# Kernel tuning notes

Hardware: AMD Instinct MI355X
Metric: run time of the kernel (lower is better)

The kernel has to match this reference:

```python
import jax, jax.numpy as jnp
import numpy as np

B, T, M, E, H = 8, 1024, 8192, 1024, 128
DECAY = 0.01
LQ_ADD = 1e-4
POS_TABLE_SIZE = 32


def setup_inputs() -> dict:
    key = jax.random.key(0)
    ks = jax.random.split(key, 9)
    return {
        "block_pos_list": jax.random.randint(ks[0], (B,), 0, 10),
        "inp": jax.random.normal(ks[1], (B, T, E), jnp.float32),
        "memory": jax.random.normal(ks[2], (B, M, E), jnp.float32),
        "memory_block_dist": jax.random.randint(ks[3], (B, M), 0, 1000).astype(jnp.int32),
        "memory_rank": jax.random.normal(ks[4], (B, M), jnp.float32),
        "pos_table": jax.random.normal(ks[5], (POS_TABLE_SIZE, E), jnp.float32) * 0.02,
        "Wk": jax.random.normal(ks[6], (H, E), jnp.float32) / np.float32(np.sqrt(E)),
        "Wq": jax.random.normal(ks[7], (H, E), jnp.float32) / np.float32(np.sqrt(E)),
        "Wv": jax.random.normal(ks[8], (H, E), jnp.float32) / np.float32(np.sqrt(E)),
    }


def reference(block_pos_list, inp, memory, memory_block_dist, memory_rank, pos_table, Wk, Wq, Wv):
    # --- reset slots where block_pos == 0 (start of a new work) ---
    reset = (block_pos_list == 0)                               # [B]
    memory = jnp.where(reset[:, None, None], 0.0, memory)       # [B, M, E]
    dist = jnp.where(reset[:, None], 0, memory_block_dist) + 1  # [B, M]

    # --- log2-bucketed positional embedding added to memory ---
    m_pos_ix = jnp.floor(jnp.log2(dist.astype(jnp.float32))).astype(jnp.int32)
    m_with_emb = memory + pos_table[m_pos_ix]                   # [B, M, E]
    mk = jnp.concatenate([m_with_emb, inp], axis=1)             # [B, M+T, E]

    # --- projections (torch Linear: x @ W.T) ---
    k = jnp.einsum('bse,he->bsh', mk, Wk)                       # [B, M+T, H]
    q = jnp.einsum('bte,he->bth', inp, Wq)                      # [B, T, H]
    v = jnp.einsum('bse,he->bsh', mk, Wv)                       # [B, M+T, H]

    # --- square + max-normalize attention (not softmax) ---
    mbs = M + T
    wei = jnp.einsum('bth,bsh->bts', q, k) * np.float32(mbs ** -0.5)  # [B, T, M+T]
    wei = wei * wei
    wei = wei / jnp.max(wei, axis=2, keepdims=True)

    # --- per-slot rank update ---
    mean_wei = jnp.mean(jnp.sum(wei, axis=1), axis=1)           # [B]
    new_rank = memory_rank + jnp.sum(wei[:, :, :M], axis=1) / mean_wei[:, None] - 1.0 - DECAY

    # --- sort memory slots by rank (descending), evict bottom block ---
    order = jnp.argsort(-new_rank, axis=1)                      # [B, M]
    mem_s = jnp.take_along_axis(memory, order[:, :, None], axis=1)
    dist_s = jnp.take_along_axis(dist, order, axis=1)
    rank_s = jnp.take_along_axis(new_rank, order, axis=1)
    r = min(T, M)
    new_memory = jax.lax.stop_gradient(mem_s.at[:, -r:].set(inp[:, -r:]))
    new_dist = dist_s.at[:, -r:].set(0)
    new_rank_out = jax.lax.stop_gradient(rank_s.at[:, -r:].set(1.0))

    qt_loss = jnp.sum(jnp.log(wei + LQ_ADD))
    out = jnp.einsum('bts,bsh->bth', wei, v)                    # [B, T, H]
    return out, qt_loss, new_memory, new_dist, new_rank_out
```

## Files before the change

kernel.cpp:

```cpp
#include <hip/hip_runtime.h>
#include <hip/hip_bf16.h>
#include <stdint.h>

#define BB 8
#define TT 1024
#define MM 8192
#define EE 1024
#define HH 128
#define SS (MM + TT)
#define RKEEP (MM - 1024)
#define NSPLIT 8
#define SCHUNK (SS / NSPLIT)
#define NT (SCHUNK / 64)
#define BK 32
#define NKVBLK (SS / 64)

typedef __attribute__((ext_vector_type(8))) short bf16x8;
typedef __attribute__((ext_vector_type(4))) short s16x4;
typedef __attribute__((ext_vector_type(4))) float f32x4;

#define SBAR()   __builtin_amdgcn_s_barrier()
#define SCB()    __builtin_amdgcn_sched_barrier(0)

static __device__ __forceinline__ unsigned f2ord(float f) {
    unsigned u = __float_as_uint(f);
    return u ^ ((u & 0x80000000u) ? 0xFFFFFFFFu : 0x80000000u);
}
static __device__ __forceinline__ float ord2f(unsigned o) {
    unsigned u = (o & 0x80000000u) ? (o ^ 0x80000000u) : ~o;
    return __uint_as_float(u);
}
static __device__ __forceinline__ unsigned short f2bf(float x) {
    unsigned u = __float_as_uint(x);
    unsigned r = u + 0x7FFFu + ((u >> 16) & 1u);
    return (unsigned short)(r >> 16);
}

static __device__ __forceinline__ void gload_lds16(const short* g, short* l) {
    __builtin_amdgcn_global_load_lds(
        (const __attribute__((address_space(1))) void*)g,
        (__attribute__((address_space(3))) void*)l, 16, 0, 0);
}

__device__ const float SCALEF = (float)(1.0 / 96.0);

__global__ __launch_bounds__(256) void k_init(
    const float* __restrict__ Wk, const float* __restrict__ Wq, const float* __restrict__ Wv,
    short* __restrict__ wk, short* __restrict__ wq, short* __restrict__ wv,
    float* __restrict__ outZ, float* __restrict__ rmax)
{
    const int blk = blockIdx.x, tid = threadIdx.x;
    if (blk < 384) {
        int idx = blk * 256 + tid;
        int m = idx >> 15;
        int o4 = (idx & 32767) * 4;
        const float* W = m == 0 ? Wk : (m == 1 ? Wq : Wv);
        short* D = m == 0 ? wk : (m == 1 ? wq : wv);
        f32x4 v = *(const f32x4*)&W[o4];
        s16x4 h;
#pragma unroll
        for (int j = 0; j < 4; ++j) h[j] = (short)f2bf(v[j]);
        *(s16x4*)&D[o4] = h;
    } else {
        const int z = (blk - 384) * 256 + tid;
        const f32x4 zero = (f32x4){0.f, 0.f, 0.f, 0.f};
        for (int i = z; i < (BB * TT * HH) / 4; i += 128 * 256)
            ((f32x4*)outZ)[i] = zero;
        if (z == 0) outZ[BB * TT * HH] = 0.f;
        if (z < (BB * TT) / 4) ((f32x4*)rmax)[z] = zero;
    }
}

__global__ __launch_bounds__(256, 4) void k_proj(
    const float* __restrict__ memory, const int* __restrict__ mbd,
    const int* __restrict__ bpl, const float* __restrict__ pos_table,
    const float* __restrict__ inp,
    const short* __restrict__ wk, const short* __restrict__ wv,
    const short* __restrict__ wq,
    short* __restrict__ kb, short* __restrict__ vT, short* __restrict__ qb)
{
    __shared__ __align__(16) short smA[64 * 64];
    __shared__ __align__(16) short smB[2][2][128 * 32];

    const int tid = threadIdx.x;
    const int b   = blockIdx.y;
    const int lane = tid & 63, wid = tid >> 6;
    const int wc = wid;
    const int fr = lane & 15, fq = lane >> 4;
    const int arow = tid >> 2;
    const int aq   = tid & 3;
    const int wh   = (tid >> 2);
    const int wk8  = (tid & 3) * 8;
    const int wdst = wid * 512;

    if (blockIdx.x < NKVBLK) {
        const int s0 = blockIdx.x * 64;
        const bool reset = (bpl[b] == 0);
        int pix;
        const float* abase;
        {
            int s = s0 + arow;
            if (s < MM) {
                int d = reset ? 1 : (mbd[b * MM + s] + 1);
                pix = 31 - __clz(d);
                abase = reset ? nullptr : &memory[((size_t)b * MM + s) * EE];
            } else {
                pix = -1;
                abase = &inp[((size_t)b * TT + (s - MM)) * EE];
            }
        }

        f32x4 accK[4][2], accV[4][2];
#pragma unroll
        for (int m = 0; m < 4; ++m)
#pragma unroll
            for (int n = 0; n < 2; ++n) {
                accK[m][n] = (f32x4){0.f, 0.f, 0.f, 0.f};
                accV[m][n] = (f32x4){0.f, 0.f, 0.f, 0.f};
            }

        auto STAGEW = [&](int e0, int buf) {
#pragma unroll
            for (int p = 0; p < 2; ++p) {
                int h = p * 64 + wh;
                int ec = wk8 ^ ((h & 3) << 3);
                size_t g = (size_t)h * EE + e0 + ec;
                gload_lds16(&wk[g], &smB[buf][0][p * 2048 + wdst]);
                gload_lds16(&wv[g], &smB[buf][1][p * 2048 + wdst]);
            }
        };
        auto LOADP = [&](int p, f32x4 xa[4]) {
            int e0 = p * 64 + aq * 16;
#pragma unroll
            for (int j = 0; j < 4; ++j) {
                f32x4 v = (f32x4){0.f, 0.f, 0.f, 0.f};
                if (abase) v = *(const f32x4*)&abase[e0 + j * 4];
                if (pix >= 0) {
                    f32x4 pt = *(const f32x4*)&pos_table[(size_t)pix * EE + e0 + j * 4];
                    v[0] += pt[0]; v[1] += pt[1]; v[2] += pt[2]; v[3] += pt[3];
                }
                xa[j] = v;
            }
        };
        auto STOREP = [&](const f32x4 xa[4]) {
#pragma unroll
            for (int j = 0; j < 2; ++j) {
                bf16x8 h;
#pragma unroll
                for (int c = 0; c < 4; ++c) {
                    h[c]     = (short)f2bf(xa[2 * j][c]);
                    h[4 + c] = (short)f2bf(xa[2 * j + 1][c]);
                }
                int g = (aq * 2 + j) ^ (arow & 7);
                *(bf16x8*)&smA[arow * 64 + g * 8] = h;
            }
        };

        f32x4 xa[4];
        LOADP(0, xa);
        STOREP(xa);
        STAGEW(0, 0);
        __syncthreads();
        LOADP(1, xa);

        for (int step = 0; step < 32; ++step) {
            const int wbuf = step & 1;
            const int sseg = step & 1;
            if (step < 31) STAGEW((step + 1) * BK, wbuf ^ 1);

            bf16x8 ah[4];
#pragma unroll
            for (int m = 0; m < 4; ++m) {
                int r = m * 16 + fr;
                int g = (sseg * 4 + fq) ^ (r & 7);
                ah[m] = *(const bf16x8*)&smA[r * 64 + g * 8];
            }
#pragma unroll
            for (int n = 0; n < 2; ++n) {
                int c = wc * 32 + n * 16 + fr;
                int off = c * 32 + ((fq * 8) ^ ((c & 3) << 3));
                bf16x8 kh = *(const bf16x8*)&smB[wbuf][0][off];
                bf16x8 vh = *(const bf16x8*)&smB[wbuf][1][off];
#pragma unroll
                for (int m = 0; m < 4; ++m) {
                    accK[m][n] = __builtin_amdgcn_mfma_f32_16x16x32_bf16(ah[m], kh, accK[m][n], 0, 0, 0);
                    accV[m][n] = __builtin_amdgcn_mfma_f32_16x16x32_bf16(ah[m], vh, accV[m][n], 0, 0, 0);
                }
            }
            __syncthreads();
            if (sseg == 1 && step < 31) {
                STOREP(xa);
                __syncthreads();
                if (step < 29) LOADP((step >> 1) + 2, xa);
            }
        }

#pragma unroll
        for (int m = 0; m < 4; ++m) {
            int row = s0 + m * 16 + fq * 4;
#pragma unroll
            for (int n = 0; n < 2; ++n) {
                int col = wc * 32 + n * 16 + fr;
#pragma unroll
                for (int i = 0; i < 4; ++i)
                    kb[((size_t)b * SS + row + i) * HH + col] = (short)f2bf(accK[m][n][i]);
            }
        }
        float* tpT = (float*)smB;
#pragma unroll
        for (int hp = 0; hp < 4; ++hp) {
            __syncthreads();
            if (wc == hp) {
#pragma unroll
                for (int m = 0; m < 4; ++m)
#pragma unroll
                    for (int n = 0; n < 2; ++n) {
                        int cl = n * 16 + fr;
                        int row = m * 16 + fq * 4;
                        *(f32x4*)&tpT[cl * 68 + row] = accV[m][n];
                    }
            }
            __syncthreads();
            for (int idx = tid; idx < 32 * 16; idx += 256) {
                int hcl = idx >> 4, s4 = (idx & 15) << 2;
                f32x4 v = *(const f32x4*)&tpT[hcl * 68 + s4];
                s16x4 hi;
#pragma unroll
                for (int j = 0; j < 4; ++j) hi[j] = (short)f2bf(v[j]);
                size_t o = ((size_t)b * HH + hp * 32 + hcl) * SS + s0 + s4;
                *(s16x4*)&vT[o] = hi;
            }
        }
    } else {
        const int t0 = (blockIdx.x - NKVBLK) * 64;
        const float* abase = &inp[((size_t)b * TT + t0 + arow) * EE];

        f32x4 acc[4][2];
#pragma unroll
        for (int m = 0; m < 4; ++m)
#pragma unroll
            for (int n = 0; n < 2; ++n) acc[m][n] = (f32x4){0.f, 0.f, 0.f, 0.f};

        auto STAGEWQ = [&](int e0, int buf) {
#pragma unroll
            for (int p = 0; p < 2; ++p) {
                int h = p * 64 + wh;
                int ec = wk8 ^ ((h & 3) << 3);
                size_t g = (size_t)h * EE + e0 + ec;
                gload_lds16(&wq[g], &smB[buf][0][p * 2048 + wdst]);
            }
        };
        auto LOADPQ = [&](int p, f32x4 xa[4]) {
            int e0 = p * 64 + aq * 16;
#pragma unroll
            for (int j = 0; j < 4; ++j) xa[j] = *(const f32x4*)&abase[e0 + j * 4];
        };
        auto STOREPQ = [&](const f32x4 xa[4]) {
#pragma unroll
            for (int j = 0; j < 2; ++j) {
                bf16x8 h;
#pragma unroll
                for (int c = 0; c < 4; ++c) {
                    h[c]     = (short)f2bf(xa[2 * j][c]);
                    h[4 + c] = (short)f2bf(xa[2 * j + 1][c]);
                }
                int g = (aq * 2 + j) ^ (arow & 7);
                *(bf16x8*)&smA[arow * 64 + g * 8] = h;
            }
        };

        f32x4 xa[4];
        LOADPQ(0, xa);
        STOREPQ(xa);
        STAGEWQ(0, 0);
        __syncthreads();
        LOADPQ(1, xa);

        for (int step = 0; step < 32; ++step) {
            const int wbuf = step & 1;
            const int sseg = step & 1;
            if (step < 31) STAGEWQ((step + 1) * BK, wbuf ^ 1);

            bf16x8 ah[4];
#pragma unroll
            for (int m = 0; m < 4; ++m) {
                int r = m * 16 + fr;
                int g = (sseg * 4 + fq) ^ (r & 7);
                ah[m] = *(const bf16x8*)&smA[r * 64 + g * 8];
            }
#pragma unroll
            for (int n = 0; n < 2; ++n) {
                int c = wc * 32 + n * 16 + fr;
                int off = c * 32 + ((fq * 8) ^ ((c & 3) << 3));
                bf16x8 bh = *(const bf16x8*)&smB[wbuf][0][off];
#pragma unroll
                for (int m = 0; m < 4; ++m)
                    acc[m][n] = __builtin_amdgcn_mfma_f32_16x16x32_bf16(ah[m], bh, acc[m][n], 0, 0, 0);
            }
            __syncthreads();
            if (sseg == 1 && step < 31) {
                STOREPQ(xa);
                __syncthreads();
                if (step < 29) LOADPQ((step >> 1) + 2, xa);
            }
        }
#pragma unroll
        for (int m = 0; m < 4; ++m) {
            int row = t0 + m * 16 + fq * 4;
#pragma unroll
            for (int n = 0; n < 2; ++n) {
                int col = wc * 32 + n * 16 + fr;
#pragma unroll
                for (int i = 0; i < 4; ++i)
                    qb[((size_t)b * TT + row + i) * HH + col] = (short)f2bf(acc[m][n][i]);
            }
        }
    }
}

__device__ __forceinline__ void stage_k64_async(const short* __restrict__ src,
                                                size_t rowBase, int tid, short* sh)
{
#pragma unroll
    for (int c2 = 0; c2 < 4; ++c2) {
        int srow = c2 * 16 + (tid >> 4);
        int scol = ((tid & 15) * 8) ^ ((srow & 7) << 3);
        size_t g = (rowBase + srow) * HH + scol;
        gload_lds16(&src[g], &sh[c2 * 2048 + (tid >> 6) * 512]);
    }
}

__device__ __forceinline__ void stage_v64_async(const short* __restrict__ vT,
                                                int b, int st, int tid, short* vs)
{
#pragma unroll
    for (int c2 = 0; c2 < 4; ++c2) {
        int h = c2 * 32 + (tid >> 3);
        int sc = ((tid & 7) * 8) ^ ((h & 7) << 3);
        size_t g = ((size_t)b * HH + h) * SS + st + sc;
        gload_lds16(&vT[g], &vs[c2 * 2048 + (tid >> 6) * 512]);
    }
}

__device__ __forceinline__ void load_qfrags(const short* __restrict__ qb,
                                            size_t rowIx, int fq, bf16x8 qh[4])
{
    size_t base = rowIx * HH + fq * 8;
#pragma unroll
    for (int k = 0; k < 4; ++k)
        qh[k] = *(const bf16x8*)&qb[base + k * 32];
}

__device__ __forceinline__ void qk_mfma4(const bf16x8 qh[4], const short* sh,
                                         int fr, int fq, f32x4 acc[4])
{
#pragma unroll
    for (int n = 0; n < 4; ++n) {
        int sc = n * 16 + fr;
        int ro = sc * 128, msk = (sc & 7) << 3;
#pragma unroll
        for (int k = 0; k < 4; ++k) {
            int off = ro + ((k * 32 + fq * 8) ^ msk);
            bf16x8 bh = *(const bf16x8*)&sh[off];
            acc[n] = __builtin_amdgcn_mfma_f32_16x16x32_bf16(qh[k], bh, acc[n], 0, 0, 0);
        }
    }
}

__device__ __forceinline__ void xcd_remap(int f, int& b, int& split, int& ttile)
{
    int xcd = f & 7, slot = f >> 3;
    int g = (slot >> 4) * 8 + xcd;
    ttile = slot & 15;
    b = g >> 3;
    split = g & 7;
}

__global__ __launch_bounds__(256) void k_rowmax(
    const short* __restrict__ qb, const short* __restrict__ kb,
    float* __restrict__ rowmax)
{
    __shared__ short Ks[2][64 * 128];
    const int tid = threadIdx.x, lane = tid & 63, wloc = tid >> 6;
    const int fr = lane & 15, fq = lane >> 4;
    int b, split, ttile;
    xcd_remap(blockIdx.x, b, split, ttile);
    const int t0 = ttile * 64;

    bf16x8 qh[4];
    load_qfrags(qb, (size_t)b * TT + t0 + wloc * 16 + fr, fq, qh);

    float rm[4] = {0.f, 0.f, 0.f, 0.f};
    const int sBeg = split * SCHUNK;
    const size_t kbase = (size_t)b * SS;

    stage_k64_async(kb, kbase + sBeg, tid, Ks[0]);
    __syncthreads();
    for (int t = 0; t < NT; ++t) {
        const int bf = t & 1;
        if (t + 1 < NT)
            stage_k64_async(kb, kbase + sBeg + (t + 1) * 64, tid, Ks[bf ^ 1]);
        f32x4 acc[4];
#pragma unroll
        for (int n = 0; n < 4; ++n) acc[n] = (f32x4){0.f, 0.f, 0.f, 0.f};
        __builtin_amdgcn_s_setprio(1);
        qk_mfma4(qh, Ks[bf], fr, fq, acc);
        __builtin_amdgcn_s_setprio(0);
#pragma unroll
        for (int n = 0; n < 4; ++n)
#pragma unroll
            for (int i = 0; i < 4; ++i) {
                float w = acc[n][i] * SCALEF;
                rm[i] = fmaxf(rm[i], w * w);
            }
        __syncthreads();
    }
#pragma unroll
    for (int d = 1; d < 16; d <<= 1)
#pragma unroll
        for (int i = 0; i < 4; ++i)
            rm[i] = fmaxf(rm[i], __shfl_xor(rm[i], d, 64));
    if (fr == 0)
#pragma unroll
        for (int i = 0; i < 4; ++i)
            atomicMax((int*)&rowmax[b * TT + t0 + wloc * 16 + fq * 4 + i], __float_as_int(rm[i]));
}

__global__ __launch_bounds__(256) void k_attn(
    const short* __restrict__ qb, const short* __restrict__ kb,
    const short* __restrict__ vT,
    const float* __restrict__ rowmax,
    float* __restrict__ outAcc, float* __restrict__ cpart, float* __restrict__ qtloss)
{
    __shared__ short Ks[2][64 * 128];
    __shared__ short Vs[2][128 * 64];
    __shared__ short Ph[64 * 64];
    __shared__ float csLDS[SCHUNK];
    __shared__ float qred[256];
    const int tid = threadIdx.x, lane = tid & 63, wloc = tid >> 6;
    const int fr = lane & 15, fq = lane >> 4;
    int b, split, ttile;
    xcd_remap(blockIdx.x, b, split, ttile);
    const int t0 = ttile * 64;

    for (int i = tid; i < SCHUNK; i += 256) csLDS[i] = 0.f;

    bf16x8 qh[4];
    load_qfrags(qb, (size_t)b * TT + t0 + wloc * 16 + fr, fq, qh);

    float inv[4];
#pragma unroll
    for (int i = 0; i < 4; ++i)
        inv[i] = 1.0f / rowmax[b * TT + t0 + wloc * 16 + fq * 4 + i];

    f32x4 oacc[8];
#pragma unroll
    for (int n = 0; n < 8; ++n) oacc[n] = (f32x4){0.f, 0.f, 0.f, 0.f};
    float qtp = 0.f;

    const int sBeg = split * SCHUNK;
    const size_t kbase = (size_t)b * SS;

    stage_k64_async(kb, kbase + sBeg, tid, Ks[0]);
    stage_v64_async(vT, b, sBeg, tid, Vs[0]);

    for (int t = 0; t < NT; ++t) {
        const int bf = t & 1;
        __syncthreads();

        if (t + 1 < NT) {
            stage_k64_async(kb, kbase + sBeg + (t + 1) * 64, tid, Ks[bf ^ 1]);
            stage_v64_async(vT, b, sBeg + (t + 1) * 64, tid, Vs[bf ^ 1]);
        }

        f32x4 acc[4];
#pragma unroll
        for (int n = 0; n < 4; ++n) acc[n] = (f32x4){0.f, 0.f, 0.f, 0.f};
        __builtin_amdgcn_s_setprio(1);
        qk_mfma4(qh, Ks[bf], fr, fq, acc);
        __builtin_amdgcn_s_setprio(0);

#pragma unroll
        for (int n = 0; n < 4; ++n) {
            float cp = 0.f;
#pragma unroll
            for (int i = 0; i < 4; ++i) {
                float w = acc[n][i] * SCALEF;
                float w2 = w * w;
                float wei = w2 * inv[i];
                qtp += __logf(wei + 1e-4f);
                cp += wei;
                int r = wloc * 16 + fq * 4 + i;
                int sw = (n * 16 + fr) ^ ((r & 7) << 3);
                Ph[r * 64 + sw] = (short)f2bf(wei);
            }
            cp += __shfl_xor(cp, 16, 64);
            cp += __shfl_xor(cp, 32, 64);
            if (fq == 0) atomicAdd(&csLDS[t * 64 + n * 16 + fr], cp);
        }
        asm volatile("s_waitcnt lgkmcnt(0)" ::: "memory");
        SBAR(); SCB();
        {
            int rA = wloc * 16 + fr;
            __builtin_amdgcn_s_setprio(1);
#pragma unroll
            for (int k = 0; k < 2; ++k) {
                int offA = rA * 64 + ((k * 32 + fq * 8) ^ ((rA & 7) << 3));
                bf16x8 ph = *(const bf16x8*)&Ph[offA];
#pragma unroll
                for (int n = 0; n < 8; ++n) {
                    int hc = n * 16 + fr;
                    int offB = hc * 64 + ((k * 32 + fq * 8) ^ ((hc & 7) << 3));
                    bf16x8 vh = *(const bf16x8*)&Vs[bf][offB];
                    oacc[n] = __builtin_amdgcn_mfma_f32_16x16x32_bf16(ph, vh, oacc[n], 0, 0, 0);
                }
            }
            __builtin_amdgcn_s_setprio(0);
        }
    }

#pragma unroll
    for (int n = 0; n < 8; ++n)
#pragma unroll
        for (int i = 0; i < 4; ++i)
            atomicAdd(&outAcc[((size_t)b * TT + t0 + wloc * 16 + fq * 4 + i) * HH + n * 16 + fr],
                      oacc[n][i]);

    qred[tid] = qtp;
    __syncthreads();
    for (int off = 128; off; off >>= 1) {
        if (tid < off) qred[tid] += qred[tid + off];
        __syncthreads();
    }
    if (tid == 0) atomicAdd(qtloss, qred[0]);

    for (int s = tid; s < SCHUNK; s += 256)
        cpart[((size_t)(b * 16 + ttile)) * SS + sBeg + s] = csLDS[s];
}

__global__ __launch_bounds__(1024) void k_ranksort(
    const float* __restrict__ cpart, const float* __restrict__ mrank,
    float* __restrict__ csum, unsigned long long* __restrict__ keys)
{
    __shared__ unsigned long long a[MM];
    __shared__ float red[1024];
    const int b = blockIdx.x, tid = threadIdx.x;

    float p = 0.f;
    for (int s = tid; s < SS; s += 1024) {
        float cs = 0.f;
#pragma unroll
        for (int tt = 0; tt < 16; ++tt) cs += cpart[((size_t)(b * 16 + tt)) * SS + s];
        csum[b * SS + s] = cs;
        p += cs;
    }
    red[tid] = p;
    __syncthreads();
    for (int off = 512; off; off >>= 1) {
        if (tid < off) red[tid] += red[tid + off];
        __syncthreads();
    }
    float mean = red[0] / (float)SS;
    for (int m = tid; m < MM; m += 1024) {
        float rank = ((mrank[b * MM + m] + csum[b * SS + m] / mean) - 1.0f) - 0.01f;
        a[m] = ((unsigned long long)(unsigned)(~f2ord(rank)) << 32) | (unsigned)m;
    }
    __syncthreads();

    for (int k = 2; k <= MM; k <<= 1) {
        for (int j = k >> 1; j > 0; j >>= 1) {
            for (int i = tid; i < MM; i += 1024) {
                int l = i ^ j;
                if (l > i) {
                    unsigned long long x = a[i], y = a[l];
                    bool up = ((i & k) == 0);
                    if ((x > y) == up) { a[i] = y; a[l] = x; }
                }
            }
            __syncthreads();
        }
    }
    for (int i = tid; i < MM; i += 1024) keys[(size_t)b * MM + i] = a[i];
}

__global__ __launch_bounds__(256) void k_scatter(
    const float* __restrict__ memory, const int* __restrict__ mbd,
    const int* __restrict__ bpl, const float* __restrict__ inp,
    const unsigned long long* __restrict__ keys,
    float* __restrict__ nmem, float* __restrict__ ndist, float* __restrict__ nrank)
{
    const int blk = blockIdx.x;
    const int b = blk >> 10;
    const int p0 = (blk & 1023) * 8;
    const bool reset = (bpl[b] == 0);
    const int tid = threadIdx.x;
    const f32x4 zero = (f32x4){0.f, 0.f, 0.f, 0.f};

    f32x4 vr[8];
    float dist[8], rankv[8];
#pragma unroll
    for (int r = 0; r < 8; ++r) {
        int p = p0 + r;
        if (p < RKEEP) {
            unsigned long long key = keys[(size_t)b * MM + p];
            int src = (int)(unsigned)(key & 0xFFFFFFFFu);
            vr[r] = reset ? zero
                          : *(const f32x4*)&memory[((size_t)b * MM + src) * EE + tid * 4];
            dist[r]  = reset ? 1.0f : (float)(mbd[b * MM + src] + 1);
            rankv[r] = ord2f(~(unsigned)(key >> 32));
        } else {
            int irow = p - RKEEP;
            vr[r] = *(const f32x4*)&inp[((size_t)b * TT + irow) * EE + tid * 4];
            dist[r] = 0.f; rankv[r] = 1.0f;
        }
    }
#pragma unroll
    for (int r = 0; r < 8; ++r) {
        int p = p0 + r;
        *(f32x4*)&nmem[((size_t)b * MM + p) * EE + tid * 4] = vr[r];
        if (tid == 0) { ndist[b * MM + p] = dist[r]; nrank[b * MM + p] = rankv[r]; }
    }
}

extern "C" void kernel_launch(void* const* d_in, const int* in_sizes, int n_in,
                              void* d_out, int out_size, void* d_ws, size_t ws_size,
                              hipStream_t stream)
{
    const int*   bpl    = (const int*)d_in[0];
    const float* inp    = (const float*)d_in[1];
    const float* memory = (const float*)d_in[2];
    const int*   mbd    = (const int*)d_in[3];
    const float* mrank  = (const float*)d_in[4];
    const float* pos    = (const float*)d_in[5];
    const float* Wk     = (const float*)d_in[6];
    const float* Wq     = (const float*)d_in[7];
    const float* Wv     = (const float*)d_in[8];

    float* out   = (float*)d_out;
    float* qtl   = out + (size_t)BB * TT * HH;
    float* nmem  = qtl + 1;
    float* ndist = nmem + (size_t)BB * MM * EE;
    float* nrank = ndist + (size_t)BB * MM;

    char* w = (char*)d_ws;
    short* qb = (short*)w; w += (size_t)BB * TT * HH * 2;
    short* kb = (short*)w; w += (size_t)BB * SS * HH * 2;
    short* vT = (short*)w; w += (size_t)BB * HH * SS * 2;
    float* rmax = (float*)w; w += (size_t)BB * TT * 4;
    float* csum = (float*)w; w += (size_t)BB * SS * 4;
    float* cpart = (float*)w; w += (size_t)BB * 16 * SS * 4;
    unsigned long long* keys = (unsigned long long*)w; w += (size_t)BB * MM * 8;
    short* wk = (short*)w; w += (size_t)HH * EE * 2;
    short* wq = (short*)w; w += (size_t)HH * EE * 2;
    short* wv = (short*)w; w += (size_t)HH * EE * 2;
    if ((size_t)(w - (char*)d_ws) > ws_size) return;

    k_init   <<<512, 256, 0, stream>>>(Wk, Wq, Wv, wk, wq, wv, out, rmax);
    k_proj   <<<dim3(NKVBLK + TT / 64, BB), 256, 0, stream>>>(memory, mbd, bpl, pos, inp,
                                                              wk, wv, wq, kb, vT, qb);
    k_rowmax <<<NSPLIT * (TT / 64) * BB, 256, 0, stream>>>(qb, kb, rmax);
    k_attn   <<<NSPLIT * (TT / 64) * BB, 256, 0, stream>>>(qb, kb, vT,
                                                           rmax, out, cpart, qtl);
    k_ranksort<<<BB, 1024, 0, stream>>>(cpart, mrank, csum, keys);
    k_scatter<<<BB * (MM / 8), 256, 0, stream>>>(memory, mbd, bpl, inp, keys, nmem, ndist, nrank);
}
```

Baseline: 523.1 us.

## Double-buffer projection A tile and overlap input-row copy with rank sort

The projection kernel now keeps two shared-memory buffers for the converted activation tile. The next tile is stored while the current one is consumed, which removes an extra barrier per pair of steps, and the occupancy hint drops from 4 to 3 to make room for the larger LDS footprint. The copy of input rows into the evicted tail of the new memory moves from the scatter kernel into extra blocks of the sort launch, so it runs concurrently with the 8-block sort. Scatter now only handles kept rows. The extra sort-launch blocks each reserve the sort's large static LDS, which may limit concurrency.

New measurement: 507.8 us. 2.9% less time.

```diff
diff --git a/kernel.cpp b/kernel.cpp
--- a/kernel.cpp
+++ b/kernel.cpp
@@ -71,7 +71,7 @@
     }
 }
 
-__global__ __launch_bounds__(256, 4) void k_proj(
+__global__ __launch_bounds__(256, 3) void k_proj(
     const float* __restrict__ memory, const int* __restrict__ mbd,
     const int* __restrict__ bpl, const float* __restrict__ pos_table,
     const float* __restrict__ inp,
@@ -79,7 +79,7 @@
     const short* __restrict__ wq,
     short* __restrict__ kb, short* __restrict__ vT, short* __restrict__ qb)
 {
-    __shared__ __align__(16) short smA[64 * 64];
+    __shared__ __align__(16) short smA[2][64 * 64];
     __shared__ __align__(16) short smB[2][2][128 * 32];
 
     const int tid = threadIdx.x;
@@ -142,7 +142,7 @@
                 xa[j] = v;
             }
         };
-        auto STOREP = [&](const f32x4 xa[4]) {
+        auto STOREP = [&](const f32x4 xa[4], int abuf) {
 #pragma unroll
             for (int j = 0; j < 2; ++j) {
                 bf16x8 h;
@@ -152,13 +152,13 @@
                     h[4 + c] = (short)f2bf(xa[2 * j + 1][c]);
                 }
                 int g = (aq * 2 + j) ^ (arow & 7);
-                *(bf16x8*)&smA[arow * 64 + g * 8] = h;
+                *(bf16x8*)&smA[abuf][arow * 64 + g * 8] = h;
             }
         };
 
         f32x4 xa[4];
         LOADP(0, xa);
-        STOREP(xa);
+        STOREP(xa, 0);
         STAGEW(0, 0);
         __syncthreads();
         LOADP(1, xa);
@@ -166,6 +166,7 @@
         for (int step = 0; step < 32; ++step) {
             const int wbuf = step & 1;
             const int sseg = step & 1;
+            const int pbuf = (step >> 1) & 1;
             if (step < 31) STAGEW((step + 1) * BK, wbuf ^ 1);
 
             bf16x8 ah[4];
@@ -173,7 +174,7 @@
             for (int m = 0; m < 4; ++m) {
                 int r = m * 16 + fr;
                 int g = (sseg * 4 + fq) ^ (r & 7);
-                ah[m] = *(const bf16x8*)&smA[r * 64 + g * 8];
+                ah[m] = *(const bf16x8*)&smA[pbuf][r * 64 + g * 8];
             }
 #pragma unroll
             for (int n = 0; n < 2; ++n) {
@@ -187,12 +188,9 @@
                     accV[m][n] = __builtin_amdgcn_mfma_f32_16x16x32_bf16(ah[m], vh, accV[m][n], 0, 0, 0);
                 }
             }
+            if (sseg == 1 && step < 31) STOREP(xa, pbuf ^ 1);
             __syncthreads();
-            if (sseg == 1 && step < 31) {
-                STOREP(xa);
-                __syncthreads();
-                if (step < 29) LOADP((step >> 1) + 2, xa);
-            }
+            if (sseg == 1 && step < 29) LOADP((step >> 1) + 2, xa);
         }
 
 #pragma unroll
@@ -255,7 +253,7 @@
 #pragma unroll
             for (int j = 0; j < 4; ++j) xa[j] = *(const f32x4*)&abase[e0 + j * 4];
         };
-        auto STOREPQ = [&](const f32x4 xa[4]) {
+        auto STOREPQ = [&](const f32x4 xa[4], int abuf) {
 #pragma unroll
             for (int j = 0; j < 2; ++j) {
                 bf16x8 h;
@@ -265,13 +263,13 @@
                     h[4 + c] = (short)f2bf(xa[2 * j + 1][c]);
                 }
                 int g = (aq * 2 + j) ^ (arow & 7);
-                *(bf16x8*)&smA[arow * 64 + g * 8] = h;
+                *(bf16x8*)&smA[abuf][arow * 64 + g * 8] = h;
             }
         };
 
         f32x4 xa[4];
         LOADPQ(0, xa);
-        STOREPQ(xa);
+        STOREPQ(xa, 0);
         STAGEWQ(0, 0);
         __syncthreads();
         LOADPQ(1, xa);
@@ -279,6 +277,7 @@
         for (int step = 0; step < 32; ++step) {
             const int wbuf = step & 1;
             const int sseg = step & 1;
+            const int pbuf = (step >> 1) & 1;
             if (step < 31) STAGEWQ((step + 1) * BK, wbuf ^ 1);
 
             bf16x8 ah[4];
@@ -286,7 +285,7 @@
             for (int m = 0; m < 4; ++m) {
                 int r = m * 16 + fr;
                 int g = (sseg * 4 + fq) ^ (r & 7);
-                ah[m] = *(const bf16x8*)&smA[r * 64 + g * 8];
+                ah[m] = *(const bf16x8*)&smA[pbuf][r * 64 + g * 8];
             }
 #pragma unroll
             for (int n = 0; n < 2; ++n) {
@@ -297,12 +296,9 @@
                 for (int m = 0; m < 4; ++m)
                     acc[m][n] = __builtin_amdgcn_mfma_f32_16x16x32_bf16(ah[m], bh, acc[m][n], 0, 0, 0);
             }
+            if (sseg == 1 && step < 31) STOREPQ(xa, pbuf ^ 1);
             __syncthreads();
-            if (sseg == 1 && step < 31) {
-                STOREPQ(xa);
-                __syncthreads();
-                if (step < 29) LOADPQ((step >> 1) + 2, xa);
-            }
+            if (sseg == 1 && step < 29) LOADPQ((step >> 1) + 2, xa);
         }
 #pragma unroll
         for (int m = 0; m < 4; ++m) {
@@ -540,12 +536,35 @@
 
 __global__ __launch_bounds__(1024) void k_ranksort(
     const float* __restrict__ cpart, const float* __restrict__ mrank,
-    float* __restrict__ csum, unsigned long long* __restrict__ keys)
+    float* __restrict__ csum, unsigned long long* __restrict__ keys,
+    const float* __restrict__ inp, float* __restrict__ nmem,
+    float* __restrict__ ndist, float* __restrict__ nrank)
 {
     __shared__ unsigned long long a[MM];
     __shared__ float red[1024];
-    const int b = blockIdx.x, tid = threadIdx.x;
-
+    const int blk = blockIdx.x, tid = threadIdx.x;
+
+    if (blk >= BB) {
+        const int idx = blk - BB;
+        const int b = idx >> 7;
+        const int r0 = RKEEP + (idx & 127) * 8;
+#pragma unroll
+        for (int rr = 0; rr < 2; ++rr) {
+            int row = r0 + rr * 4 + (tid >> 8);
+            int irow = row - RKEEP;
+            int c4 = (tid & 255) * 4;
+            *(f32x4*)&nmem[((size_t)b * MM + row) * EE + c4] =
+                *(const f32x4*)&inp[((size_t)b * TT + irow) * EE + c4];
+        }
+        if (tid < 8) {
+            int p = r0 + tid;
+            ndist[b * MM + p] = 0.f;
+            nrank[b * MM + p] = 1.0f;
+        }
+        return;
+    }
+
+    const int b = blk;
     float p = 0.f;
     for (int s = tid; s < SS; s += 1024) {
         float cs = 0.f;
@@ -585,13 +604,12 @@
 
 __global__ __launch_bounds__(256) void k_scatter(
     const float* __restrict__ memory, const int* __restrict__ mbd,
-    const int* __restrict__ bpl, const float* __restrict__ inp,
-    const unsigned long long* __restrict__ keys,
+    const int* __restrict__ bpl, const unsigned long long* __restrict__ keys,
     float* __restrict__ nmem, float* __restrict__ ndist, float* __restrict__ nrank)
 {
     const int blk = blockIdx.x;
-    const int b = blk >> 10;
-    const int p0 = (blk & 1023) * 8;
+    const int b = blk / (RKEEP / 8);
+    const int p0 = (blk % (RKEEP / 8)) * 8;
     const bool reset = (bpl[b] == 0);
     const int tid = threadIdx.x;
     const f32x4 zero = (f32x4){0.f, 0.f, 0.f, 0.f};
@@ -601,18 +619,12 @@
 #pragma unroll
     for (int r = 0; r < 8; ++r) {
         int p = p0 + r;
-        if (p < RKEEP) {
-            unsigned long long key = keys[(size_t)b * MM + p];
-            int src = (int)(unsigned)(key & 0xFFFFFFFFu);
-            vr[r] = reset ? zero
-                          : *(const f32x4*)&memory[((size_t)b * MM + src) * EE + tid * 4];
-            dist[r]  = reset ? 1.0f : (float)(mbd[b * MM + src] + 1);
-            rankv[r] = ord2f(~(unsigned)(key >> 32));
-        } else {
-            int irow = p - RKEEP;
-            vr[r] = *(const f32x4*)&inp[((size_t)b * TT + irow) * EE + tid * 4];
-            dist[r] = 0.f; rankv[r] = 1.0f;
-        }
+        unsigned long long key = keys[(size_t)b * MM + p];
+        int src = (int)(unsigned)(key & 0xFFFFFFFFu);
+        vr[r] = reset ? zero
+                      : *(const f32x4*)&memory[((size_t)b * MM + src) * EE + tid * 4];
+        dist[r]  = reset ? 1.0f : (float)(mbd[b * MM + src] + 1);
+        rankv[r] = ord2f(~(unsigned)(key >> 32));
     }
 #pragma unroll
     for (int r = 0; r < 8; ++r) {
@@ -661,6 +673,8 @@
     k_rowmax <<<NSPLIT * (TT / 64) * BB, 256, 0, stream>>>(qb, kb, rmax);
     k_attn   <<<NSPLIT * (TT / 64) * BB, 256, 0, stream>>>(qb, kb, vT,
                                                            rmax, out, cpart, qtl);
-    k_ranksort<<<BB, 1024, 0, stream>>>(cpart, mrank, csum, keys);
-    k_scatter<<<BB * (MM / 8), 256, 0, stream>>>(memory, mbd, bpl, inp, keys, nmem, ndist, nrank);
-}
+    k_ranksort<<<BB + BB * 128, 1024, 0, stream>>>(cpart, mrank, csum, keys,
+                                                   inp, nmem, ndist, nrank);
+    k_scatter<<<BB * (RKEEP / 8), 256, 0, stream>>>(memory, mbd, bpl, keys,
+                                                    nmem, ndist, nrank);
+}
```
